# Kernel optimization log

Hardware: AMD Instinct MI355X
Metric: run time of the kernel (lower is better)

## Reference

```python
import jax, jax.numpy as jnp
import numpy as np

HEADS = 8
DIM_HEAD = 64
SCALE = DIM_HEAD ** -0.5
POS_DIM = 64


def _sincos_pe(H, W, dim, dtype):
    # matches build_2d_sincos_pos_embed: [1, dim, H, W]
    y = jnp.linspace(-1.0, 1.0, H)[:, None] * jnp.ones((1, W), jnp.float32)
    x = jnp.ones((H, 1), jnp.float32) * jnp.linspace(-1.0, 1.0, W)[None, :]
    omega = 1.0 / (10000.0 ** (jnp.arange(dim // 4, dtype=jnp.float32) / (dim // 4)))
    px = x[..., None] * omega  # [H, W, dim//4]
    py = y[..., None] * omega
    pe = jnp.concatenate([jnp.sin(px), jnp.cos(px), jnp.sin(py), jnp.cos(py)], axis=-1)
    return pe.transpose(2, 0, 1)[None].astype(dtype)


def _conv2d(x, w):
    return jax.lax.conv_general_dilated(
        x, w, (1, 1), 'SAME', dimension_numbers=('NCHW', 'OIHW', 'NCHW'))


def _sobel(d):
    kx = jnp.array([[1, 0, -1], [2, 0, -2], [1, 0, -1]], jnp.float32).reshape(1, 1, 3, 3)
    ky = jnp.array([[1, 2, 1], [0, 0, 0], [-1, -2, -1]], jnp.float32).reshape(1, 1, 3, 3)
    return _conv2d(d, kx), _conv2d(d, ky)


def setup_inputs() -> dict:
    key = jax.random.key(0)
    ks = jax.random.split(key, 8)
    B, C, H, W = 2, 256, 64, 64
    hid = HEADS * DIM_HEAD  # 512
    s = 0.02
    return {
        'x': jax.random.normal(ks[0], (B, C, H, W), jnp.float32),
        'dsm': jax.random.uniform(ks[1], (B, 1, H, W), jnp.float32),
        'wq': jax.random.normal(ks[2], (hid, C), jnp.float32) * s,
        'wkv': jax.random.normal(ks[3], (2 * hid, C + 1), jnp.float32) * s,
        'wout': jax.random.normal(ks[4], (C, hid), jnp.float32) * s,
        'bout': jnp.zeros((C,), jnp.float32),
        'w_hape': jax.random.normal(ks[5], (hid, POS_DIM + 3), jnp.float32) * s,
        'b_hape': jnp.zeros((hid,), jnp.float32),
        'w_alpha': jax.random.normal(ks[6], (1, 1, 3, 3), jnp.float32) * 0.1,
        'b_alpha': jnp.zeros((1,), jnp.float32),
    }


def reference(x, dsm, wq, wkv, wout, bout, w_hape, b_hape, w_alpha, b_alpha):
    B, C, H, W = x.shape
    hid = wq.shape[0]
    # per-sample min-max normalize DSM over spatial dims
    dmin = dsm.min(axis=(2, 3), keepdims=True)
    dmax = dsm.max(axis=(2, 3), keepdims=True)
    d = (dsm - dmin) / (dmax - dmin + 1e-6)
    # HAPE: [PE | h | grad_h] -> 1x1 conv to hidden
    pe = jnp.broadcast_to(_sincos_pe(H, W, POS_DIM, x.dtype), (B, POS_DIM, H, W))
    gx, gy = _sobel(d)
    hape_in = jnp.concatenate([pe, d, gx, gy], axis=1)  # [B, 67, H, W]
    hape_k = jnp.einsum('oc,bchw->bohw', w_hape, hape_in) + b_hape[None, :, None, None]
    # QKV via 1x1 convs
    q = jnp.einsum('oc,bchw->bohw', wq, x)
    kv = jnp.einsum('oc,bchw->bohw', wkv, jnp.concatenate([x, d], axis=1))
    k = kv[:, :hid] + hape_k
    v = kv[:, hid:]
    to_heads = lambda t: t.reshape(B, HEADS, DIM_HEAD, H * W)  # b (h c) x y -> b h c (xy)
    qh = to_heads(q) * SCALE
    kh = to_heads(k)
    vh = to_heads(v)
    sim = jnp.einsum('bhdi,bhdj->bhij', qh, kh)  # [B, h, N, N]
    attn = jax.nn.softmax(sim, axis=-1)
    out = jnp.einsum('bhij,bhdj->bhid', attn, vh)  # [B, h, N, d]
    # b h (x y) d -> b (h d) x y
    out = out.transpose(0, 1, 3, 2).reshape(B, HEADS * DIM_HEAD, H, W)
    out = jnp.einsum('oc,bchw->bohw', wout, out) + bout[None, :, None, None]
    # fine: gradient-magnitude alpha gating
    mag = jnp.sqrt(jnp.maximum(gx, 0.0) ** 2 + jnp.maximum(gy, 0.0) ** 2 + 1e-12)
    alpha = jax.nn.sigmoid(_conv2d(mag, w_alpha) + b_alpha[None, :, None, None])
    return x + out * alpha
```

## Files before the change

kernel.cpp:

```cpp
#include <hip/hip_runtime.h>
#include <math.h>

#define NPOS 4096
#define MTOT 8192
#define KP   352
#define HT 64
#define WT 64
#define NSPLIT 2
#define KEYS_PER (NPOS / NSPLIT)
#define NCH (KEYS_PER / 64)

typedef unsigned short ushortT;
typedef short v8s __attribute__((ext_vector_type(8)));
typedef float v4f __attribute__((ext_vector_type(4)));
typedef unsigned uint2v __attribute__((ext_vector_type(2)));

static __device__ __forceinline__ ushortT bfr(float f) {
    union { float f; unsigned u; } v; v.f = f;
    return (ushortT)((v.u + 0x8000u) >> 16);
}
static __device__ __forceinline__ unsigned pack2bf(float a, float b) {
    union { float f; unsigned u; } ua, ub; ua.f = a; ub.f = b;
    return __builtin_amdgcn_perm(ub.u + 0x8000u, ua.u + 0x8000u, 0x07060302u);
}
static __device__ __forceinline__ unsigned pack2bf_t(float a, float b) {
    union { float f; unsigned u; } ua, ub; ua.f = a; ub.f = b;
    return __builtin_amdgcn_perm(ub.u, ua.u, 0x07060302u);
}
static __device__ __forceinline__ float fexp2(float x) {
#if __has_builtin(__builtin_amdgcn_exp2f)
    return __builtin_amdgcn_exp2f(x);
#else
    return exp2f(x);
#endif
}

__global__ void k_minmax(const float* __restrict__ dsm, float* __restrict__ mm) {
    int b = blockIdx.x;
    const float* p = dsm + (size_t)b * NPOS;
    float mn = 1e30f, mx = -1e30f;
    for (int i = threadIdx.x; i < NPOS; i += 256) {
        float v = p[i];
        mn = fminf(mn, v); mx = fmaxf(mx, v);
    }
    for (int off = 32; off; off >>= 1) {
        mn = fminf(mn, __shfl_xor(mn, off, 64));
        mx = fmaxf(mx, __shfl_xor(mx, off, 64));
    }
    __shared__ float smn[4], smx[4];
    int wid = threadIdx.x >> 6;
    if ((threadIdx.x & 63) == 0) { smn[wid] = mn; smx[wid] = mx; }
    __syncthreads();
    if (threadIdx.x == 0) {
        mn = fminf(fminf(smn[0], smn[1]), fminf(smn[2], smn[3]));
        mx = fmaxf(fmaxf(smx[0], smx[1]), fmaxf(smx[2], smx[3]));
        mm[b * 2 + 0] = mn; mm[b * 2 + 1] = mx;
    }
}

__global__ void k_prep(const float* __restrict__ dsm, const float* __restrict__ mm,
                       const float* __restrict__ walpha, const float* __restrict__ balpha,
                       ushortT* __restrict__ F, float* __restrict__ alpha) {
    int idx = blockIdx.x * 256 + threadIdx.x;
    int b = idx / NPOS, n = idx % NPOS;
    int hh = n / WT, ww = n % WT;
    float dmin = mm[b * 2], dmax = mm[b * 2 + 1];
    float inv = 1.0f / (dmax - dmin + 1e-6f);
    const float* dp = dsm + (size_t)b * NPOS;

    float dwin[5][5];
    #pragma unroll
    for (int dy = 0; dy < 5; dy++)
        #pragma unroll
        for (int dx = 0; dx < 5; dx++) {
            int y = hh + dy - 2, x = ww + dx - 2;
            float v = 0.0f;
            if (y >= 0 && y < HT && x >= 0 && x < WT) v = (dp[y * WT + x] - dmin) * inv;
            dwin[dy][dx] = v;
        }

    float gxc = 0.f, gyc = 0.f;
    float conv = 0.f;
    #pragma unroll
    for (int oy = 0; oy < 3; oy++)
        #pragma unroll
        for (int ox = 0; ox < 3; ox++) {
            int qy = hh + oy - 1, qx = ww + ox - 1;
            float m = 0.0f;
            if (qy >= 0 && qy < HT && qx >= 0 && qx < WT) {
                float gx = dwin[oy][ox] - dwin[oy][ox + 2]
                         + 2.f * dwin[oy + 1][ox] - 2.f * dwin[oy + 1][ox + 2]
                         + dwin[oy + 2][ox] - dwin[oy + 2][ox + 2];
                float gy = dwin[oy][ox] + 2.f * dwin[oy][ox + 1] + dwin[oy][ox + 2]
                         - dwin[oy + 2][ox] - 2.f * dwin[oy + 2][ox + 1] - dwin[oy + 2][ox + 2];
                if (oy == 1 && ox == 1) { gxc = gx; gyc = gy; }
                float rx = fmaxf(gx, 0.f), ry = fmaxf(gy, 0.f);
                m = sqrtf(rx * rx + ry * ry + 1e-12f);
            }
            conv += walpha[oy * 3 + ox] * m;
        }
    alpha[idx] = 1.f / (1.f + __expf(-(conv + balpha[0])));

    ushortT* fb = F + (size_t)idx * KP;
    fb[256] = bfr(dwin[2][2]);
    fb[257] = bfr(gxc);
    fb[258] = bfr(gyc);
    float xc = -1.f + 2.f * (float)ww / 63.f;
    float yc = -1.f + 2.f * (float)hh / 63.f;
    const float l2w = 13.287712379549449f;
    #pragma unroll
    for (int i = 0; i < 16; i++) {
        float omega = exp2f(-(float)i * (l2w / 16.f));
        float px = xc * omega, py = yc * omega;
        fb[259 + i]      = bfr(__sinf(px));
        fb[259 + 16 + i] = bfr(__cosf(px));
        fb[259 + 32 + i] = bfr(__sinf(py));
        fb[259 + 48 + i] = bfr(__cosf(py));
    }
    #pragma unroll
    for (int z = 323; z < KP; z++) fb[z] = 0;
}

__global__ void k_cast(const float* __restrict__ x, ushortT* __restrict__ F) {
    __shared__ __align__(16) ushortT Tl[64][72];
    int nt = blockIdx.x * 64;
    int b = blockIdx.y >> 2, ct = (blockIdx.y & 3) * 64;
    int t = threadIdx.x;
    #pragma unroll
    for (int rep = 0; rep < 4; rep++) {
        int row = rep * 16 + (t >> 4), c4 = (t & 15) * 4;
        float4 f4 = *(const float4*)&x[((size_t)(b * 256 + ct + row)) * NPOS + nt + c4];
        Tl[c4 + 0][row] = bfr(f4.x);
        Tl[c4 + 1][row] = bfr(f4.y);
        Tl[c4 + 2][row] = bfr(f4.z);
        Tl[c4 + 3][row] = bfr(f4.w);
    }
    __syncthreads();
    #pragma unroll
    for (int rep = 0; rep < 2; rep++) {
        int slot = rep * 256 + t, row = slot >> 3, c8 = slot & 7;
        *(uint4*)&F[((size_t)(b * 4096 + nt + row)) * KP + ct + c8 * 8] = *(uint4*)&Tl[row][c8 * 8];
    }
}

__global__ void k_wcprep(const float* __restrict__ wq, const float* __restrict__ wkv,
                         const float* __restrict__ whape, const float* __restrict__ bhape,
                         ushortT* __restrict__ Wc, float* __restrict__ biasc) {
    int idx = blockIdx.x * 256 + threadIdx.x;
    int o = idx / KP, k = idx % KP;
    float v = 0.f;
    if (o < 512) {
        if (k < 256) v = wq[o * 256 + k] * 0.18033688011112042f;
        if (k == 0) biasc[o] = 0.f;
    } else if (o < 1024) {
        int r = o - 512;
        if (k < 257) v = wkv[r * 257 + k];
        if (k == 256)      v += whape[r * 67 + 64];
        else if (k == 257) v = whape[r * 67 + 65];
        else if (k == 258) v = whape[r * 67 + 66];
        else if (k >= 259 && k < 323) v = whape[r * 67 + (k - 259)];
        if (k == 0) biasc[o] = bhape[r];
    } else {
        int r = o - 512;
        if (k < 257) v = wkv[r * 257 + k];
        if (k == 0) biasc[o] = 0.f;
    }
    Wc[idx] = bfr(v);
}

__global__ void k_wout(const float* __restrict__ wout, ushortT* __restrict__ woutb) {
    int idx = blockIdx.x * 256 + threadIdx.x;
    woutb[idx] = bfr(wout[idx]);
}

__global__ __launch_bounds__(256) void k_gemm1(const ushortT* __restrict__ Wc, const ushortT* __restrict__ F,
                                               const float* __restrict__ biasc,
                                               ushortT* __restrict__ qT, ushortT* __restrict__ kT,
                                               ushortT* __restrict__ vv) {
    __shared__ __align__(16) ushortT Al[64][40];
    __shared__ __align__(16) ushortT Bl[64][40];
    __shared__ __align__(16) ushortT Vt[64][72];
    int mt = blockIdx.x * 64;
    int ot = blockIdx.y * 64;
    int t = threadIdx.x, w = t >> 6, lane = t & 63, u = lane & 15, quad = lane >> 4;
    int arow = t >> 2, ac8 = t & 3;
    v4f acc[4] = {};
    for (int k0 = 0; k0 < KP; k0 += 32) {
        __syncthreads();
        *(uint4*)&Al[arow][ac8 * 8] = *(const uint4*)&Wc[(size_t)(ot + arow) * KP + k0 + ac8 * 8];
        *(uint4*)&Bl[arow][ac8 * 8] = *(const uint4*)&F[(size_t)(mt + arow) * KP + k0 + ac8 * 8];
        __syncthreads();
        v8s a = *(v8s*)&Al[w * 16 + u][quad * 8];
        #pragma unroll
        for (int n4 = 0; n4 < 4; n4++) {
            v8s bb = *(v8s*)&Bl[n4 * 16 + u][quad * 8];
            acc[n4] = __builtin_amdgcn_mfma_f32_16x16x32_bf16(a, bb, acc[n4], 0, 0, 0);
        }
    }
    int obase = ot + w * 16 + quad * 4;
    float bo[4];
    #pragma unroll
    for (int r = 0; r < 4; r++) bo[r] = biasc[obase + r];
    if (ot < 1024) {
        int h = (ot >> 6) & 7;
        ushortT* dst = (ot < 512) ? qT : kT;
        #pragma unroll
        for (int n4 = 0; n4 < 4; n4++) {
            int m = mt + n4 * 16 + u;
            uint2 val;
            val.x = pack2bf(acc[n4][0] + bo[0], acc[n4][1] + bo[1]);
            val.y = pack2bf(acc[n4][2] + bo[2], acc[n4][3] + bo[3]);
            *(uint2*)&dst[((size_t)h * MTOT + m) * 64 + w * 16 + quad * 4] = val;
        }
    } else {
        __syncthreads();
        #pragma unroll
        for (int n4 = 0; n4 < 4; n4++) {
            int ml = n4 * 16 + u;
            #pragma unroll
            for (int r = 0; r < 4; r++) Vt[w * 16 + quad * 4 + r][ml] = bfr(acc[n4][r] + bo[r]);
        }
        __syncthreads();
        #pragma unroll
        for (int rep = 0; rep < 2; rep++) {
            int slot = rep * 256 + t, row = slot >> 3, c8 = slot & 7;
            *(uint4*)&vv[(size_t)(ot - 1024 + row) * MTOT + mt + c8 * 8] = *(uint4*)&Vt[row][c8 * 8];
        }
    }
}

#define LIDX(row, cb) (((row) << 6) + ((((cb) ^ ((row) & 7))) << 3))
__global__ __launch_bounds__(256, 3) void k_flash(const ushortT* __restrict__ qT,
                                                  const ushortT* __restrict__ kT,
                                                  const ushortT* __restrict__ vv,
                                                  float* __restrict__ Opart,
                                                  float* __restrict__ liPart) {
    __shared__ __align__(16) ushortT Kbuf[2][64 * 64];
    __shared__ __align__(16) ushortT Vbuf[2][64 * 64];

    int it = blockIdx.x;
    int bh = blockIdx.y;
    int half = blockIdx.z;
    int b = bh >> 3, h = bh & 7;
    int colbase = b * NPOS;
    int t = threadIdx.x, w = t >> 6, lane = t & 63, u = lane & 15, quad = lane >> 4;
    int qb = it * 128 + w * 32;

    const ushortT* Qg = qT + ((size_t)h * MTOT + colbase + qb) * 64;
    const ushortT* Kg = kT + ((size_t)h * MTOT + colbase + half * KEYS_PER) * 64;
    const ushortT* Vg = vv + ((size_t)(h * 64)) * MTOT + colbase + half * KEYS_PER;

    int row0 = t >> 3,        c80 = t & 7;
    int row1 = (256 + t) >> 3, c81 = t & 7;

    v8s bq[2][2];
    #pragma unroll
    for (int g = 0; g < 2; g++)
        #pragma unroll
        for (int hf = 0; hf < 2; hf++)
            bq[g][hf] = *(const v8s*)&Qg[(size_t)(g * 16 + u) * 64 + hf * 32 + quad * 8];

    float li[2] = {0.f, 0.f};
    v4f O[4][2] = {};

    uint4 kr0 = *(const uint4*)&Kg[(size_t)row0 * 64 + c80 * 8];
    uint4 kr1 = *(const uint4*)&Kg[(size_t)row1 * 64 + c81 * 8];
    uint4 vr0 = *(const uint4*)&Vg[(size_t)row0 * MTOT + c80 * 8];
    uint4 vr1 = *(const uint4*)&Vg[(size_t)row1 * MTOT + c81 * 8];

    for (int jc = 0; jc < NCH; jc++) {
        int cur = jc & 1;
        *(uint4*)&Kbuf[cur][LIDX(row0, c80)] = kr0;
        *(uint4*)&Kbuf[cur][LIDX(row1, c81)] = kr1;
        *(uint4*)&Vbuf[cur][LIDX(row0, c80)] = vr0;
        *(uint4*)&Vbuf[cur][LIDX(row1, c81)] = vr1;
        if (jc + 1 < NCH) {
            int jb = (jc + 1) * 64;
            kr0 = *(const uint4*)&Kg[(size_t)(jb + row0) * 64 + c80 * 8];
            kr1 = *(const uint4*)&Kg[(size_t)(jb + row1) * 64 + c81 * 8];
            vr0 = *(const uint4*)&Vg[(size_t)row0 * MTOT + jb + c80 * 8];
            vr1 = *(const uint4*)&Vg[(size_t)row1 * MTOT + jb + c81 * 8];
        }
        __syncthreads();

        const ushortT* Kb = &Kbuf[cur][0];
        const ushortT* Vb = &Vbuf[cur][0];

        v8s bp[2][2];
        #pragma unroll
        for (int kp = 0; kp < 2; kp++) {
            unsigned pk0[2][2], pk1[2][2];
            #pragma unroll
            for (int kk = 0; kk < 2; kk++) {
                int k4 = kp * 2 + kk;
                v8s ak0 = *(const v8s*)&Kb[LIDX(k4 * 16 + u, quad)];
                v8s ak1 = *(const v8s*)&Kb[LIDX(k4 * 16 + u, 4 + quad)];
                v4f st[2];
                #pragma unroll
                for (int g = 0; g < 2; g++) {
                    st[g] = (v4f){0.f, 0.f, 0.f, 0.f};
                    st[g] = __builtin_amdgcn_mfma_f32_16x16x32_bf16(ak0, bq[g][0], st[g], 0, 0, 0);
                    st[g] = __builtin_amdgcn_mfma_f32_16x16x32_bf16(ak1, bq[g][1], st[g], 0, 0, 0);
                }
                #pragma unroll
                for (int g = 0; g < 2; g++) {
                    float p0 = fexp2(st[g][0]);
                    float p1 = fexp2(st[g][1]);
                    float p2 = fexp2(st[g][2]);
                    float p3 = fexp2(st[g][3]);
                    li[g] += (p0 + p1) + (p2 + p3);
                    pk0[g][kk] = pack2bf_t(p0, p1);
                    pk1[g][kk] = pack2bf_t(p2, p3);
                }
            }
            #pragma unroll
            for (int g = 0; g < 2; g++) {
                uint2v r0 = __builtin_amdgcn_permlane32_swap(pk0[g][0], pk0[g][1], false, false);
                uint2v r1 = __builtin_amdgcn_permlane32_swap(pk1[g][0], pk1[g][1], false, false);
                uint2v t0 = __builtin_amdgcn_permlane16_swap(r0.x, r0.y, false, false);
                uint2v t1 = __builtin_amdgcn_permlane16_swap(r1.x, r1.y, false, false);
                union { uint4 u4; v8s s; } cv;
                cv.u4.x = t0.x; cv.u4.y = t1.x; cv.u4.z = t0.y; cv.u4.w = t1.y;
                bp[g][kp] = cv.s;
            }
        }

        #pragma unroll
        for (int d4 = 0; d4 < 4; d4++) {
            v8s av0 = *(const v8s*)&Vb[LIDX(d4 * 16 + u, quad)];
            v8s av1 = *(const v8s*)&Vb[LIDX(d4 * 16 + u, 4 + quad)];
            #pragma unroll
            for (int g = 0; g < 2; g++) {
                O[d4][g] = __builtin_amdgcn_mfma_f32_16x16x32_bf16(av0, bp[g][0], O[d4][g], 0, 0, 0);
                O[d4][g] = __builtin_amdgcn_mfma_f32_16x16x32_bf16(av1, bp[g][1], O[d4][g], 0, 0, 0);
            }
        }
    }

    #pragma unroll
    for (int g = 0; g < 2; g++) {
        li[g] += __shfl_xor(li[g], 16, 64);
        li[g] += __shfl_xor(li[g], 32, 64);
        int q = qb + g * 16 + u;
        size_t m2 = (size_t)(half * 2 + b) * 4096 + q;
        size_t base = m2 * 512 + h * 64;
        #pragma unroll
        for (int d4 = 0; d4 < 4; d4++) {
            float4 o4;
            o4.x = O[d4][g][0]; o4.y = O[d4][g][1]; o4.z = O[d4][g][2]; o4.w = O[d4][g][3];
            *(float4*)&Opart[base + d4 * 16 + quad * 4] = o4;
        }
        if (quad == 0) liPart[m2 * 8 + h] = li[g];
    }
}

__global__ __launch_bounds__(256) void k_comb(const float* __restrict__ Opart,
                                              const float* __restrict__ liPart,
                                              ushortT* __restrict__ aoB) {
    int tid = blockIdx.x * 256 + threadIdx.x;
    int m = tid >> 7, c4 = (tid & 127) * 4, h = c4 >> 6;
    float l = 0.f;
    #pragma unroll
    for (int s = 0; s < NSPLIT; s++) l += liPart[((size_t)s * 8192 + m) * 8 + h];
    float inv = 1.f / l;
    float ox = 0.f, oy = 0.f, oz = 0.f, ow = 0.f;
    #pragma unroll
    for (int s = 0; s < NSPLIT; s++) {
        float4 o = *(const float4*)&Opart[((size_t)s * 8192 + m) * 512 + c4];
        ox += o.x; oy += o.y; oz += o.z; ow += o.w;
    }
    uint2 val;
    val.x = pack2bf(ox * inv, oy * inv);
    val.y = pack2bf(oz * inv, ow * inv);
    *(uint2*)&aoB[(size_t)m * 512 + c4] = val;
}

__global__ __launch_bounds__(256) void k_gemm2(const ushortT* __restrict__ woutb, const ushortT* __restrict__ aoB,
                                               const float* __restrict__ bout, const float* __restrict__ x,
                                               const float* __restrict__ alpha, float* __restrict__ out) {
    __shared__ __align__(16) ushortT Al[64][40];
    __shared__ __align__(16) ushortT Bl[64][40];
    int mt = blockIdx.x * 64;
    int ot = blockIdx.y * 64;
    int t = threadIdx.x, w = t >> 6, lane = t & 63, u = lane & 15, quad = lane >> 4;
    int arow = t >> 2, ac8 = t & 3;
    v4f acc[4] = {};
    for (int k0 = 0; k0 < 512; k0 += 32) {
        __syncthreads();
        *(uint4*)&Al[arow][ac8 * 8] = *(const uint4*)&woutb[(size_t)(ot + arow) * 512 + k0 + ac8 * 8];
        *(uint4*)&Bl[arow][ac8 * 8] = *(const uint4*)&aoB[(size_t)(mt + arow) * 512 + k0 + ac8 * 8];
        __syncthreads();
        v8s a = *(v8s*)&Al[w * 16 + u][quad * 8];
        #pragma unroll
        for (int n4 = 0; n4 < 4; n4++) {
            v8s bb = *(v8s*)&Bl[n4 * 16 + u][quad * 8];
            acc[n4] = __builtin_amdgcn_mfma_f32_16x16x32_bf16(a, bb, acc[n4], 0, 0, 0);
        }
    }
    int b = mt >> 12, n0 = mt & 4095;
    int obase = ot + w * 16 + quad * 4;
    float bo[4];
    #pragma unroll
    for (int r = 0; r < 4; r++) bo[r] = bout[obase + r];
    #pragma unroll
    for (int n4 = 0; n4 < 4; n4++) {
        int n = n0 + n4 * 16 + u;
        float al = alpha[(size_t)b * NPOS + n];
        #pragma unroll
        for (int r = 0; r < 4; r++) {
            size_t xi = ((size_t)(b * 256 + obase + r)) * NPOS + n;
            out[xi] = x[xi] + (acc[n4][r] + bo[r]) * al;
        }
    }
}

extern "C" void kernel_launch(void* const* d_in, const int* in_sizes, int n_in,
                              void* d_out, int out_size, void* d_ws, size_t ws_size,
                              hipStream_t stream) {
    const float* x      = (const float*)d_in[0];
    const float* dsm    = (const float*)d_in[1];
    const float* wq     = (const float*)d_in[2];
    const float* wkv    = (const float*)d_in[3];
    const float* wout   = (const float*)d_in[4];
    const float* bout   = (const float*)d_in[5];
    const float* whape  = (const float*)d_in[6];
    const float* bhape  = (const float*)d_in[7];
    const float* walpha = (const float*)d_in[8];
    const float* balpha = (const float*)d_in[9];
    float* out = (float*)d_out;
    float* ws  = (float*)d_ws;

    size_t off = 0;
    float* mm    = ws + off; off += 256;
    float* alpha = ws + off; off += (size_t)2 * NPOS;
    float* biasc = ws + off; off += 2048;
    float* Opart  = ws + off; off += (size_t)NSPLIT * MTOT * 512;
    float* liPart = ws + off; off += (size_t)NSPLIT * MTOT * 8;
    ushortT* F     = (ushortT*)(ws + off); off += (size_t)MTOT * KP / 2;
    ushortT* Wc    = (ushortT*)(ws + off); off += (size_t)1536 * KP / 2;
    ushortT* woutb = (ushortT*)(ws + off); off += (size_t)256 * 512 / 2;
    ushortT* qT    = (ushortT*)(ws + off); off += (size_t)8 * MTOT * 64 / 2;
    ushortT* kT    = (ushortT*)(ws + off); off += (size_t)8 * MTOT * 64 / 2;
    ushortT* vv    = (ushortT*)(ws + off); off += (size_t)512 * MTOT / 2;
    ushortT* aoB   = (ushortT*)(ws + off); off += (size_t)MTOT * 512 / 2;
    (void)in_sizes; (void)n_in; (void)out_size; (void)ws_size;

    k_minmax<<<2, 256, 0, stream>>>(dsm, mm);
    k_prep<<<32, 256, 0, stream>>>(dsm, mm, walpha, balpha, F, alpha);
    k_cast<<<dim3(64, 8), 256, 0, stream>>>(x, F);
    k_wcprep<<<(1536 * KP) / 256, 256, 0, stream>>>(wq, wkv, whape, bhape, Wc, biasc);
    k_wout<<<512, 256, 0, stream>>>(wout, woutb);
    k_gemm1<<<dim3(128, 24), 256, 0, stream>>>(Wc, F, biasc, qT, kT, vv);
    k_flash<<<dim3(32, 16, NSPLIT), 256, 0, stream>>>(qT, kT, vv, Opart, liPart);
    k_comb<<<4096, 256, 0, stream>>>(Opart, liPart, aoB);
    k_gemm2<<<dim3(128, 4), 256, 0, stream>>>(woutb, aoB, bout, x, alpha, out);
}
```

Measured before the change: 215.1 us.

## Use direct global-to-LDS loads in flash attention, compute row sums via MFMA, fuse prep kernels

In the flash kernel, K/V tiles now go straight from global memory into LDS with global_load_lds. This drops the register staging and the explicit LDS stores, and the single barrier moves to the top of each iteration. The per-row softmax denominator is now an MFMA against a ones vector instead of scalar adds plus cross-lane shuffles, and the occupancy hint of 3 blocks per SIMD is removed. Separately, the min/max reduction is folded into k_prep (each block recomputes it redundantly) and the wout cast is folded into k_wcprep, which cuts two launches. The async LDS load path relies on implicit waits before the barrier, and the extra MFMAs add matrix work.

```diff
diff --git a/kernel.cpp b/kernel.cpp
--- a/kernel.cpp
+++ b/kernel.cpp
@@ -34,39 +34,35 @@
     return exp2f(x);
 #endif
 }
-
-__global__ void k_minmax(const float* __restrict__ dsm, float* __restrict__ mm) {
-    int b = blockIdx.x;
-    const float* p = dsm + (size_t)b * NPOS;
-    float mn = 1e30f, mx = -1e30f;
-    for (int i = threadIdx.x; i < NPOS; i += 256) {
-        float v = p[i];
-        mn = fminf(mn, v); mx = fmaxf(mx, v);
-    }
-    for (int off = 32; off; off >>= 1) {
-        mn = fminf(mn, __shfl_xor(mn, off, 64));
-        mx = fmaxf(mx, __shfl_xor(mx, off, 64));
-    }
-    __shared__ float smn[4], smx[4];
-    int wid = threadIdx.x >> 6;
-    if ((threadIdx.x & 63) == 0) { smn[wid] = mn; smx[wid] = mx; }
-    __syncthreads();
-    if (threadIdx.x == 0) {
-        mn = fminf(fminf(smn[0], smn[1]), fminf(smn[2], smn[3]));
-        mx = fmaxf(fmaxf(smx[0], smx[1]), fmaxf(smx[2], smx[3]));
-        mm[b * 2 + 0] = mn; mm[b * 2 + 1] = mx;
-    }
-}
-
-__global__ void k_prep(const float* __restrict__ dsm, const float* __restrict__ mm,
+static __device__ __forceinline__ void gll16(const ushortT* g, ushortT* l) {
+    __builtin_amdgcn_global_load_lds((const __attribute__((address_space(1))) void*)g,
+                                     (__attribute__((address_space(3))) void*)l, 16, 0, 0);
+}
+
+__global__ void k_prep(const float* __restrict__ dsm,
                        const float* __restrict__ walpha, const float* __restrict__ balpha,
                        ushortT* __restrict__ F, float* __restrict__ alpha) {
     int idx = blockIdx.x * 256 + threadIdx.x;
     int b = idx / NPOS, n = idx % NPOS;
     int hh = n / WT, ww = n % WT;
-    float dmin = mm[b * 2], dmax = mm[b * 2 + 1];
+    const float* dp = dsm + (size_t)b * NPOS;
+
+    float mn = 1e30f, mx = -1e30f;
+    for (int i = threadIdx.x; i < NPOS; i += 256) {
+        float v = dp[i];
+        mn = fminf(mn, v); mx = fmaxf(mx, v);
+    }
+    for (int off = 32; off; off >>= 1) {
+        mn = fminf(mn, __shfl_xor(mn, off, 64));
+        mx = fmaxf(mx, __shfl_xor(mx, off, 64));
+    }
+    __shared__ float smn[4], smx[4];
+    int wid = threadIdx.x >> 6;
+    if ((threadIdx.x & 63) == 0) { smn[wid] = mn; smx[wid] = mx; }
+    __syncthreads();
+    float dmin = fminf(fminf(smn[0], smn[1]), fminf(smn[2], smn[3]));
+    float dmax = fmaxf(fmaxf(smx[0], smx[1]), fmaxf(smx[2], smx[3]));
     float inv = 1.0f / (dmax - dmin + 1e-6f);
-    const float* dp = dsm + (size_t)b * NPOS;
 
     float dwin[5][5];
     #pragma unroll
@@ -145,8 +141,13 @@
 
 __global__ void k_wcprep(const float* __restrict__ wq, const float* __restrict__ wkv,
                          const float* __restrict__ whape, const float* __restrict__ bhape,
-                         ushortT* __restrict__ Wc, float* __restrict__ biasc) {
+                         const float* __restrict__ wout,
+                         ushortT* __restrict__ Wc, float* __restrict__ biasc,
+                         ushortT* __restrict__ woutb) {
     int idx = blockIdx.x * 256 + threadIdx.x;
+    if (blockIdx.x < 512) {
+        woutb[idx] = bfr(wout[idx]);
+    }
     int o = idx / KP, k = idx % KP;
     float v = 0.f;
     if (o < 512) {
@@ -168,11 +169,6 @@
     Wc[idx] = bfr(v);
 }
 
-__global__ void k_wout(const float* __restrict__ wout, ushortT* __restrict__ woutb) {
-    int idx = blockIdx.x * 256 + threadIdx.x;
-    woutb[idx] = bfr(wout[idx]);
-}
-
 __global__ __launch_bounds__(256) void k_gemm1(const ushortT* __restrict__ Wc, const ushortT* __restrict__ F,
                                                const float* __restrict__ biasc,
                                                ushortT* __restrict__ qT, ushortT* __restrict__ kT,
@@ -230,11 +226,11 @@
 }
 
 #define LIDX(row, cb) (((row) << 6) + ((((cb) ^ ((row) & 7))) << 3))
-__global__ __launch_bounds__(256, 3) void k_flash(const ushortT* __restrict__ qT,
-                                                  const ushortT* __restrict__ kT,
-                                                  const ushortT* __restrict__ vv,
-                                                  float* __restrict__ Opart,
-                                                  float* __restrict__ liPart) {
+__global__ __launch_bounds__(256) void k_flash(const ushortT* __restrict__ qT,
+                                               const ushortT* __restrict__ kT,
+                                               const ushortT* __restrict__ vv,
+                                               float* __restrict__ Opart,
+                                               float* __restrict__ liPart) {
     __shared__ __align__(16) ushortT Kbuf[2][64 * 64];
     __shared__ __align__(16) ushortT Vbuf[2][64 * 64];
 
@@ -250,8 +246,14 @@
     const ushortT* Kg = kT + ((size_t)h * MTOT + colbase + half * KEYS_PER) * 64;
     const ushortT* Vg = vv + ((size_t)(h * 64)) * MTOT + colbase + half * KEYS_PER;
 
-    int row0 = t >> 3,        c80 = t & 7;
-    int row1 = (256 + t) >> 3, c81 = t & 7;
+    int r0 = t >> 3,         c0 = (t & 7) ^ (r0 & 7);
+    int r1 = (256 + t) >> 3, c1 = (t & 7) ^ (r1 & 7);
+    const ushortT* ks0 = Kg + r0 * 64 + c0 * 8;
+    const ushortT* ks1 = Kg + r1 * 64 + c1 * 8;
+    const ushortT* vs0 = Vg + (size_t)r0 * MTOT + c0 * 8;
+    const ushortT* vs1 = Vg + (size_t)r1 * MTOT + c1 * 8;
+    ushortT* kd0 = &Kbuf[0][0] + w * 512;
+    ushortT* vd0 = &Vbuf[0][0] + w * 512;
 
     v8s bq[2][2];
     #pragma unroll
@@ -260,28 +262,30 @@
         for (int hf = 0; hf < 2; hf++)
             bq[g][hf] = *(const v8s*)&Qg[(size_t)(g * 16 + u) * 64 + hf * 32 + quad * 8];
 
-    float li[2] = {0.f, 0.f};
+    v8s ones;
+    #pragma unroll
+    for (int i = 0; i < 8; i++) ones[i] = (short)0x3F80;
+
+    v4f li4[2] = {};
     v4f O[4][2] = {};
 
-    uint4 kr0 = *(const uint4*)&Kg[(size_t)row0 * 64 + c80 * 8];
-    uint4 kr1 = *(const uint4*)&Kg[(size_t)row1 * 64 + c81 * 8];
-    uint4 vr0 = *(const uint4*)&Vg[(size_t)row0 * MTOT + c80 * 8];
-    uint4 vr1 = *(const uint4*)&Vg[(size_t)row1 * MTOT + c81 * 8];
+    gll16(ks0, kd0);
+    gll16(ks1, kd0 + 2048);
+    gll16(vs0, vd0);
+    gll16(vs1, vd0 + 2048);
 
     for (int jc = 0; jc < NCH; jc++) {
         int cur = jc & 1;
-        *(uint4*)&Kbuf[cur][LIDX(row0, c80)] = kr0;
-        *(uint4*)&Kbuf[cur][LIDX(row1, c81)] = kr1;
-        *(uint4*)&Vbuf[cur][LIDX(row0, c80)] = vr0;
-        *(uint4*)&Vbuf[cur][LIDX(row1, c81)] = vr1;
+        __syncthreads();
         if (jc + 1 < NCH) {
-            int jb = (jc + 1) * 64;
-            kr0 = *(const uint4*)&Kg[(size_t)(jb + row0) * 64 + c80 * 8];
-            kr1 = *(const uint4*)&Kg[(size_t)(jb + row1) * 64 + c81 * 8];
-            vr0 = *(const uint4*)&Vg[(size_t)row0 * MTOT + jb + c80 * 8];
-            vr1 = *(const uint4*)&Vg[(size_t)row1 * MTOT + jb + c81 * 8];
-        }
-        __syncthreads();
+            ushortT* kn = kd0 + (cur ^ 1) * 4096;
+            ushortT* vn = vd0 + (cur ^ 1) * 4096;
+            gll16(ks0 + 4096, kn);
+            gll16(ks1 + 4096, kn + 2048);
+            gll16(vs0 + 64,   vn);
+            gll16(vs1 + 64,   vn + 2048);
+            ks0 += 4096; ks1 += 4096; vs0 += 64; vs1 += 64;
+        }
 
         const ushortT* Kb = &Kbuf[cur][0];
         const ushortT* Vb = &Vbuf[cur][0];
@@ -308,21 +312,26 @@
                     float p1 = fexp2(st[g][1]);
                     float p2 = fexp2(st[g][2]);
                     float p3 = fexp2(st[g][3]);
-                    li[g] += (p0 + p1) + (p2 + p3);
                     pk0[g][kk] = pack2bf_t(p0, p1);
                     pk1[g][kk] = pack2bf_t(p2, p3);
                 }
             }
             #pragma unroll
             for (int g = 0; g < 2; g++) {
-                uint2v r0 = __builtin_amdgcn_permlane32_swap(pk0[g][0], pk0[g][1], false, false);
-                uint2v r1 = __builtin_amdgcn_permlane32_swap(pk1[g][0], pk1[g][1], false, false);
-                uint2v t0 = __builtin_amdgcn_permlane16_swap(r0.x, r0.y, false, false);
-                uint2v t1 = __builtin_amdgcn_permlane16_swap(r1.x, r1.y, false, false);
+                uint2v r0s = __builtin_amdgcn_permlane32_swap(pk0[g][0], pk0[g][1], false, false);
+                uint2v r1s = __builtin_amdgcn_permlane32_swap(pk1[g][0], pk1[g][1], false, false);
+                uint2v t0 = __builtin_amdgcn_permlane16_swap(r0s.x, r0s.y, false, false);
+                uint2v t1 = __builtin_amdgcn_permlane16_swap(r1s.x, r1s.y, false, false);
                 union { uint4 u4; v8s s; } cv;
                 cv.u4.x = t0.x; cv.u4.y = t1.x; cv.u4.z = t0.y; cv.u4.w = t1.y;
                 bp[g][kp] = cv.s;
             }
+        }
+
+        #pragma unroll
+        for (int g = 0; g < 2; g++) {
+            li4[g] = __builtin_amdgcn_mfma_f32_16x16x32_bf16(ones, bp[g][0], li4[g], 0, 0, 0);
+            li4[g] = __builtin_amdgcn_mfma_f32_16x16x32_bf16(ones, bp[g][1], li4[g], 0, 0, 0);
         }
 
         #pragma unroll
@@ -339,8 +348,6 @@
 
     #pragma unroll
     for (int g = 0; g < 2; g++) {
-        li[g] += __shfl_xor(li[g], 16, 64);
-        li[g] += __shfl_xor(li[g], 32, 64);
         int q = qb + g * 16 + u;
         size_t m2 = (size_t)(half * 2 + b) * 4096 + q;
         size_t base = m2 * 512 + h * 64;
@@ -350,7 +357,7 @@
             o4.x = O[d4][g][0]; o4.y = O[d4][g][1]; o4.z = O[d4][g][2]; o4.w = O[d4][g][3];
             *(float4*)&Opart[base + d4 * 16 + quad * 4] = o4;
         }
-        if (quad == 0) liPart[m2 * 8 + h] = li[g];
+        if (quad == 0) liPart[m2 * 8 + h] = li4[g][0];
     }
 }
 
@@ -431,7 +438,6 @@
     float* ws  = (float*)d_ws;
 
     size_t off = 0;
-    float* mm    = ws + off; off += 256;
     float* alpha = ws + off; off += (size_t)2 * NPOS;
     float* biasc = ws + off; off += 2048;
     float* Opart  = ws + off; off += (size_t)NSPLIT * MTOT * 512;
@@ -445,11 +451,9 @@
     ushortT* aoB   = (ushortT*)(ws + off); off += (size_t)MTOT * 512 / 2;
     (void)in_sizes; (void)n_in; (void)out_size; (void)ws_size;
 
-    k_minmax<<<2, 256, 0, stream>>>(dsm, mm);
-    k_prep<<<32, 256, 0, stream>>>(dsm, mm, walpha, balpha, F, alpha);
+    k_prep<<<32, 256, 0, stream>>>(dsm, walpha, balpha, F, alpha);
     k_cast<<<dim3(64, 8), 256, 0, stream>>>(x, F);
-    k_wcprep<<<(1536 * KP) / 256, 256, 0, stream>>>(wq, wkv, whape, bhape, Wc, biasc);
-    k_wout<<<512, 256, 0, stream>>>(wout, woutb);
+    k_wcprep<<<(1536 * KP) / 256, 256, 0, stream>>>(wq, wkv, whape, bhape, wout, Wc, biasc, woutb);
     k_gemm1<<<dim3(128, 24), 256, 0, stream>>>(Wc, F, biasc, qT, kT, vv);
     k_flash<<<dim3(32, 16, NSPLIT), 256, 0, stream>>>(qT, kT, vv, Opart, liPart);
     k_comb<<<4096, 256, 0, stream>>>(Opart, liPart, aoB);
```

Result: no change. 214.2 us (-0.4%).
